# Kernel optimization log

Measured on AMD Instinct MI355X. Metric: run time of the kernel, lower is better.

The kernel has to match this reference:

```python
import jax, jax.numpy as jnp
import numpy as np

B, C, D = 16, 512, 256
K = 16        # spatio_topk
RD = 128      # rec_dim
H = 8         # num_heads
FFN = 1024    # temporal_ffn
TEMP = 0.5    # temperature


def setup_inputs() -> dict:
    key = jax.random.key(0)
    ks = jax.random.split(key, 8)
    s = lambda k, shape: (jax.random.normal(k, shape, jnp.float32) * 0.02)
    return dict(
        x=jax.random.normal(ks[0], (B, C, D), jnp.float32),
        wq_rec=s(ks[1], (RD, D)),
        wk_rec=s(ks[2], (RD, D)),
        in_proj_w=s(ks[3], (3 * D, D)),
        in_proj_b=jnp.zeros((3 * D,), jnp.float32),
        out_w=s(ks[4], (D, D)),
        out_b=jnp.zeros((D,), jnp.float32),
        ln1_g=jnp.ones((D,), jnp.float32),
        ln1_b=jnp.zeros((D,), jnp.float32),
        mlp_w1=s(ks[5], (FFN, D)),
        mlp_b1=jnp.zeros((FFN,), jnp.float32),
        mlp_w2=s(ks[6], (D, FFN)),
        mlp_b2=jnp.zeros((D,), jnp.float32),
        ln2_g=jnp.ones((D,), jnp.float32),
        ln2_b=jnp.zeros((D,), jnp.float32),
    )


def _ln(x, g, b, eps=1e-5):
    m = x.mean(-1, keepdims=True)
    v = ((x - m) ** 2).mean(-1, keepdims=True)
    return (x - m) * jax.lax.rsqrt(v + eps) * g + b


def reference(x, wq_rec, wk_rec, in_proj_w, in_proj_b, out_w, out_b,
              ln1_g, ln1_b, mlp_w1, mlp_b1, mlp_w2, mlp_b2, ln2_g, ln2_b):
    b, c, d = x.shape
    # --- ST_Rec_Module (training branch: straight-through top-k routing) ---
    xq = x @ wq_rec.T                                   # (B,C,RD)
    xk = x @ wk_rec.T
    logits = jnp.einsum('bqd,bkd->bqk', xq, xk) / TEMP  # (B,C,C)
    idx = jax.lax.top_k(logits, K)[1]                   # (B,C,K)
    z_hard = jax.nn.one_hot(idx, c, dtype=x.dtype)      # (B,C,K,C)
    # cumulative mask of previously-selected channels (exclusive cumsum)
    prev = jnp.cumsum(z_hard, axis=2)
    prev = jnp.concatenate([jnp.zeros_like(prev[:, :, :1]), prev[:, :, :-1]], axis=2)
    mask = prev > 0
    zs = jnp.where(mask, -1e30, logits[:, :, None, :] / TEMP)  # logits/temp twice, as in source
    z_soft = jax.nn.softmax(zs, axis=-1)
    z = z_hard + z_soft - jax.lax.stop_gradient(z_soft)        # straight-through
    rec_x = jnp.einsum('bqkc,bcd->bqkd', z, x)                 # (B,C,K,D)

    # --- ST_Channel_Module: per-channel cross-attention, query length 1 ---
    hd = d // H
    wq, wk, wv = in_proj_w[:d], in_proj_w[d:2 * d], in_proj_w[2 * d:]
    bq, bk, bv = in_proj_b[:d], in_proj_b[d:2 * d], in_proj_b[2 * d:]
    q = (x @ wq.T + bq).reshape(b, c, H, hd)                   # (B,C,H,hd)
    k = (rec_x @ wk.T + bk).reshape(b, c, K, H, hd)
    v = (rec_x @ wv.T + bv).reshape(b, c, K, H, hd)
    scores = jnp.einsum('bchd,bckhd->bchk', q, k) / np.float32(np.sqrt(hd))
    attn = jax.nn.softmax(scores, axis=-1)
    ctx = jnp.einsum('bchk,bckhd->bchd', attn, v).reshape(b, c, d)
    attn_out = ctx @ out_w.T + out_b
    x1 = _ln(attn_out + x, ln1_g, ln1_b)

    # --- ST_Temporal_Module (Identity projections, gelu FFN + LN) ---
    h = jax.nn.gelu(x1 @ mlp_w1.T + mlp_b1, approximate=False)
    h = h @ mlp_w2.T + mlp_b2
    x2 = _ln(h + x1, ln2_g, ln2_b)
    return x2
```

## Files before the change

### kernel.cpp

```cpp
#include <hip/hip_runtime.h>
#include <hip/hip_bf16.h>
#include <math.h>

#define B_   16
#define C_   512
#define D_   256
#define K_   16
#define RD_  128
#define H_   8
#define HD_  32
#define FFN_ 1024
#define M_   (B_ * C_)

typedef __attribute__((ext_vector_type(8))) short bf16x8;
typedef __attribute__((ext_vector_type(4))) float f32x4;

typedef __attribute__((address_space(1))) const int ga_int;
typedef __attribute__((address_space(3))) int ls_int;

static __device__ __forceinline__ short f2bf(float v) {
    __hip_bfloat16 h = __float2bfloat16(v);
    return *(short*)&h;
}
static __device__ __forceinline__ float bf2f(short s) {
    __hip_bfloat16 h = *(__hip_bfloat16*)&s;
    return __bfloat162float(h);
}
static __device__ __forceinline__ float4 ld4bf(const short* p) {
    uint2 u = *(const uint2*)p;
    float4 r;
    r.x = __uint_as_float((u.x & 0xffffu) << 16);
    r.y = __uint_as_float(u.x & 0xffff0000u);
    r.z = __uint_as_float((u.y & 0xffffu) << 16);
    r.w = __uint_as_float(u.y & 0xffff0000u);
    return r;
}

#define N8_X    (M_ * D_ / 8)
#define N8_INW  (768 * D_ / 8)
#define N8_OUTW (D_ * D_ / 8)
#define N8_W1   (FFN_ * D_ / 8)
#define N8_W2   (D_ * FFN_ / 8)
#define N8_WQ   (RD_ * D_ / 8)
#define N8_ALL  (N8_X + N8_INW + N8_OUTW + N8_W1 + N8_W2 + 2 * N8_WQ)

__global__ __launch_bounds__(256) void convert_all_kernel(
    const float* __restrict__ x, const float* __restrict__ inw,
    const float* __restrict__ outw, const float* __restrict__ w1,
    const float* __restrict__ w2, const float* __restrict__ wq,
    const float* __restrict__ wk,
    short* __restrict__ xbf, short* __restrict__ xlo,
    short* __restrict__ inwbf, short* __restrict__ outwbf,
    short* __restrict__ w1bf, short* __restrict__ w2bf,
    short* __restrict__ wqh, short* __restrict__ wql,
    short* __restrict__ wkh, short* __restrict__ wkl)
{
    int i = blockIdx.x * 256 + threadIdx.x;
    if (i >= N8_ALL) return;

    const float* s; short* dh; short* dl = nullptr; int off;
    if      (i < N8_X)                    { s = x;    dh = xbf;    dl = xlo; off = i; }
    else if (i < N8_X + N8_INW)           { s = inw;  dh = inwbf;  off = i - N8_X; }
    else if (i < N8_X + N8_INW + N8_OUTW) { s = outw; dh = outwbf; off = i - N8_X - N8_INW; }
    else if (i < N8_X + N8_INW + N8_OUTW + N8_W1)
                                          { s = w1;   dh = w1bf;   off = i - N8_X - N8_INW - N8_OUTW; }
    else if (i < N8_X + N8_INW + N8_OUTW + N8_W1 + N8_W2)
                                          { s = w2;   dh = w2bf;   off = i - N8_X - N8_INW - N8_OUTW - N8_W1; }
    else if (i < N8_X + N8_INW + N8_OUTW + N8_W1 + N8_W2 + N8_WQ)
                                          { s = wq;   dh = wqh; dl = wql; off = i - N8_X - N8_INW - N8_OUTW - N8_W1 - N8_W2; }
    else                                  { s = wk;   dh = wkh; dl = wkl; off = i - N8_X - N8_INW - N8_OUTW - N8_W1 - N8_W2 - N8_WQ; }

    const float4* sp = (const float4*)s + (size_t)off * 2;
    float4 v0 = sp[0], v1 = sp[1];
    float f[8] = {v0.x, v0.y, v0.z, v0.w, v1.x, v1.y, v1.z, v1.w};
    short rh[8], rl[8];
    #pragma unroll
    for (int j = 0; j < 8; ++j) {
        rh[j] = f2bf(f[j]);
        rl[j] = f2bf(f[j] - bf2f(rh[j]));
    }
    *(bf16x8*)(dh + (size_t)off * 8) = *(bf16x8*)rh;
    if (dl) *(bf16x8*)(dl + (size_t)off * 8) = *(bf16x8*)rl;
}

template<int BM, int BN, int OUT_BF16, int ACT>
__global__ __launch_bounds__(256) void gemm_mfma(
    const short* __restrict__ A, const short* __restrict__ W,
    const float* __restrict__ bias, void* __restrict__ Cout,
    int M, int N, int Kd)
{
    __shared__ short As[2][BM * 32];
    __shared__ short Bs[2][BN * 32];
    const int tid  = threadIdx.x;
    const int wave = tid >> 6;
    const int lane = tid & 63;
    const int bm = blockIdx.y * BM;
    const int bn = blockIdx.x * BN;
    constexpr int MI = BM / 32;
    constexpr int NJ = BN / 32;
    const int wr = (wave >> 1) * (BM / 2);
    const int wc = (wave & 1) * (BN / 2);

    const int fr = lane & 15;
    const int fk = (lane >> 4) * 8;
    const int r0 = tid >> 2, ch = (tid & 3) * 8;

    f32x4 acc[MI][NJ];
    #pragma unroll
    for (int i = 0; i < MI; ++i)
        #pragma unroll
        for (int j = 0; j < NJ; ++j)
            acc[i][j] = (f32x4){0.f, 0.f, 0.f, 0.f};

    auto stage = [&](int buf, int k0) {
        #pragma unroll
        for (int i = 0; i < BM / 64; ++i)
            __builtin_amdgcn_global_load_lds(
                (ga_int*)&A[(size_t)(bm + r0 + i * 64) * Kd + k0 + ch],
                (ls_int*)&As[buf][(tid + i * 256) * 8], 16, 0, 0);
        #pragma unroll
        for (int j = 0; j < BN / 64; ++j)
            __builtin_amdgcn_global_load_lds(
                (ga_int*)&W[(size_t)(bn + r0 + j * 64) * Kd + k0 + ch],
                (ls_int*)&Bs[buf][(tid + j * 256) * 8], 16, 0, 0);
    };

    stage(0, 0);
    int cur = 0;

    for (int k0 = 0; k0 < Kd; k0 += 32) {
        __syncthreads();
        if (k0 + 32 < Kd) stage(cur ^ 1, k0 + 32);

        bf16x8 af[MI], bfr[NJ];
        #pragma unroll
        for (int i = 0; i < MI; ++i) af[i]  = *(bf16x8*)&As[cur][(wr + i * 16 + fr) * 32 + fk];
        #pragma unroll
        for (int j = 0; j < NJ; ++j) bfr[j] = *(bf16x8*)&Bs[cur][(wc + j * 16 + fr) * 32 + fk];
        #pragma unroll
        for (int i = 0; i < MI; ++i)
            #pragma unroll
            for (int j = 0; j < NJ; ++j)
                acc[i][j] = __builtin_amdgcn_mfma_f32_16x16x32_bf16(af[i], bfr[j], acc[i][j], 0, 0, 0);
        cur ^= 1;
    }

    const int rowbase = (lane >> 4) * 4;
    #pragma unroll
    for (int i = 0; i < MI; ++i) {
        #pragma unroll
        for (int j = 0; j < NJ; ++j) {
            const int n = bn + wc + j * 16 + fr;
            const float bn_v = bias ? bias[n] : 0.f;
            #pragma unroll
            for (int r = 0; r < 4; ++r) {
                const int m = bm + wr + i * 16 + rowbase + r;
                float v = acc[i][j][r] + bn_v;
                if (ACT) v = 0.5f * v * (1.0f + erff(v * 0.70710678118654752f));
                if (OUT_BF16) ((short*)Cout)[(size_t)m * N + n] = f2bf(v);
                else          ((float*)Cout)[(size_t)m * N + n] = v;
            }
        }
    }
}

__global__ __launch_bounds__(256) void proj_kernel(
    const short* __restrict__ xbf, const short* __restrict__ xlo,
    const short* __restrict__ inwbf, const float* __restrict__ in_b,
    const short* __restrict__ wqh, const short* __restrict__ wql,
    const short* __restrict__ wkh, const short* __restrict__ wkl,
    short* __restrict__ qkvbf,
    short* __restrict__ qh, short* __restrict__ ql,
    short* __restrict__ kh, short* __restrict__ kl)
{
    __shared__ short smem[12288];
    const int bid  = blockIdx.x;
    const int tid  = threadIdx.x;
    const int wave = tid >> 6;
    const int lane = tid & 63;
    const int fr = lane & 15;
    const int fk = (lane >> 4) * 8;
    const int r0 = tid >> 2, ch = (tid & 3) * 8;

    if (bid < 768) {
        const int bm = (bid / 6) * 64;
        const int bn = (bid % 6) * 128;
        const int wr = (wave >> 1) * 32;
        const int wc = (wave & 1) * 64;
        short* As = smem;
        short* Bs = smem + 4096;

        f32x4 acc[2][4];
        #pragma unroll
        for (int i = 0; i < 2; ++i)
            #pragma unroll
            for (int j = 0; j < 4; ++j)
                acc[i][j] = (f32x4){0.f, 0.f, 0.f, 0.f};

        auto stage = [&](int buf, int k0) {
            __builtin_amdgcn_global_load_lds(
                (ga_int*)&xbf[(size_t)(bm + r0) * D_ + k0 + ch],
                (ls_int*)&As[buf * 2048 + tid * 8], 16, 0, 0);
            #pragma unroll
            for (int j = 0; j < 2; ++j)
                __builtin_amdgcn_global_load_lds(
                    (ga_int*)&inwbf[(size_t)(bn + r0 + j * 64) * D_ + k0 + ch],
                    (ls_int*)&Bs[buf * 4096 + (tid + j * 256) * 8], 16, 0, 0);
        };

        stage(0, 0);
        int cur = 0;
        for (int k0 = 0; k0 < D_; k0 += 32) {
            __syncthreads();
            if (k0 + 32 < D_) stage(cur ^ 1, k0 + 32);
            bf16x8 af[2], bfr[4];
            #pragma unroll
            for (int i = 0; i < 2; ++i) af[i]  = *(bf16x8*)&As[cur * 2048 + (wr + i * 16 + fr) * 32 + fk];
            #pragma unroll
            for (int j = 0; j < 4; ++j) bfr[j] = *(bf16x8*)&Bs[cur * 4096 + (wc + j * 16 + fr) * 32 + fk];
            #pragma unroll
            for (int i = 0; i < 2; ++i)
                #pragma unroll
                for (int j = 0; j < 4; ++j)
                    acc[i][j] = __builtin_amdgcn_mfma_f32_16x16x32_bf16(af[i], bfr[j], acc[i][j], 0, 0, 0);
            cur ^= 1;
        }

        const int rowbase = (lane >> 4) * 4;
        #pragma unroll
        for (int i = 0; i < 2; ++i)
            #pragma unroll
            for (int j = 0; j < 4; ++j) {
                const int n = bn + wc + j * 16 + fr;
                const float bv = in_b[n];
                #pragma unroll
                for (int r = 0; r < 4; ++r) {
                    const int m = bm + wr + i * 16 + rowbase + r;
                    qkvbf[(size_t)m * 768 + n] = f2bf(acc[i][j][r] + bv);
                }
            }
    } else {
        const int t = bid - 768;
        const int z = t >> 8;
        const int rem = t & 255;
        const int bm = (rem >> 1) * 64;
        const int bn = (rem & 1) * 64;
        const short* Wh = z ? wkh : wqh;
        const short* Wl = z ? wkl : wql;
        short* Oh = z ? kh : qh;
        short* Ol = z ? kl : ql;
        short* Ah = smem;
        short* Al = smem + 2048;
        short* Bh = smem + 4096;
        short* Bl = smem + 6144;

        const int wr = (wave >> 1) * 32;
        const int wc = (wave & 1) * 32;

        f32x4 acc[2][2];
        #pragma unroll
        for (int i = 0; i < 2; ++i)
            #pragma unroll
            for (int j = 0; j < 2; ++j)
                acc[i][j] = (f32x4){0.f, 0.f, 0.f, 0.f};

        for (int k0 = 0; k0 < D_; k0 += 32) {
            __builtin_amdgcn_global_load_lds((ga_int*)&xbf[(size_t)(bm + r0) * D_ + k0 + ch], (ls_int*)&Ah[tid * 8], 16, 0, 0);
            __builtin_amdgcn_global_load_lds((ga_int*)&xlo[(size_t)(bm + r0) * D_ + k0 + ch], (ls_int*)&Al[tid * 8], 16, 0, 0);
            __builtin_amdgcn_global_load_lds((ga_int*)&Wh[(size_t)(bn + r0) * D_ + k0 + ch], (ls_int*)&Bh[tid * 8], 16, 0, 0);
            __builtin_amdgcn_global_load_lds((ga_int*)&Wl[(size_t)(bn + r0) * D_ + k0 + ch], (ls_int*)&Bl[tid * 8], 16, 0, 0);
            __syncthreads();

            bf16x8 ah[2], al[2], bh[2], bl[2];
            #pragma unroll
            for (int i = 0; i < 2; ++i) {
                ah[i] = *(bf16x8*)&Ah[(wr + i * 16 + fr) * 32 + fk];
                al[i] = *(bf16x8*)&Al[(wr + i * 16 + fr) * 32 + fk];
            }
            #pragma unroll
            for (int j = 0; j < 2; ++j) {
                bh[j] = *(bf16x8*)&Bh[(wc + j * 16 + fr) * 32 + fk];
                bl[j] = *(bf16x8*)&Bl[(wc + j * 16 + fr) * 32 + fk];
            }
            #pragma unroll
            for (int i = 0; i < 2; ++i)
                #pragma unroll
                for (int j = 0; j < 2; ++j) {
                    acc[i][j] = __builtin_amdgcn_mfma_f32_16x16x32_bf16(ah[i], bh[j], acc[i][j], 0, 0, 0);
                    acc[i][j] = __builtin_amdgcn_mfma_f32_16x16x32_bf16(ah[i], bl[j], acc[i][j], 0, 0, 0);
                    acc[i][j] = __builtin_amdgcn_mfma_f32_16x16x32_bf16(al[i], bh[j], acc[i][j], 0, 0, 0);
                }
            __syncthreads();
        }

        const int rowbase = (lane >> 4) * 4;
        #pragma unroll
        for (int i = 0; i < 2; ++i)
            #pragma unroll
            for (int j = 0; j < 2; ++j) {
                const int n = bn + wc + j * 16 + fr;
                #pragma unroll
                for (int r = 0; r < 4; ++r) {
                    const int m = bm + wr + i * 16 + rowbase + r;
                    float v = acc[i][j][r];
                    short h = f2bf(v);
                    Oh[(size_t)m * RD_ + n] = h;
                    Ol[(size_t)m * RD_ + n] = f2bf(v - bf2f(h));
                }
            }
    }
}

__global__ __launch_bounds__(256) void logits_mfma(
    const short* __restrict__ qh, const short* __restrict__ ql,
    const short* __restrict__ kh, const short* __restrict__ kl,
    float* __restrict__ out)
{
    __shared__ short Ah[64 * 32], Al[64 * 32], Bh[64 * 32], Bl[64 * 32];
    const int tid  = threadIdx.x;
    const int wave = tid >> 6;
    const int lane = tid & 63;
    const int base = blockIdx.z * C_;
    const int bm = blockIdx.y * 64;
    const int bn = blockIdx.x * 64;
    const int wr = (wave >> 1) * 32;
    const int wc = (wave & 1) * 32;
    const int fr = lane & 15;
    const int fk = (lane >> 4) * 8;
    const int r0 = tid >> 2, ch = (tid & 3) * 8;

    f32x4 acc[2][2];
    #pragma unroll
    for (int i = 0; i < 2; ++i)
        #pragma unroll
        for (int j = 0; j < 2; ++j)
            acc[i][j] = (f32x4){0.f, 0.f, 0.f, 0.f};

    for (int k0 = 0; k0 < RD_; k0 += 32) {
        __builtin_amdgcn_global_load_lds((ga_int*)&qh[(size_t)(base + bm + r0) * RD_ + k0 + ch], (ls_int*)&Ah[tid * 8], 16, 0, 0);
        __builtin_amdgcn_global_load_lds((ga_int*)&ql[(size_t)(base + bm + r0) * RD_ + k0 + ch], (ls_int*)&Al[tid * 8], 16, 0, 0);
        __builtin_amdgcn_global_load_lds((ga_int*)&kh[(size_t)(base + bn + r0) * RD_ + k0 + ch], (ls_int*)&Bh[tid * 8], 16, 0, 0);
        __builtin_amdgcn_global_load_lds((ga_int*)&kl[(size_t)(base + bn + r0) * RD_ + k0 + ch], (ls_int*)&Bl[tid * 8], 16, 0, 0);
        __syncthreads();

        bf16x8 ah[2], al[2], bh[2], bl[2];
        #pragma unroll
        for (int i = 0; i < 2; ++i) {
            ah[i] = *(bf16x8*)&Ah[(wr + i * 16 + fr) * 32 + fk];
            al[i] = *(bf16x8*)&Al[(wr + i * 16 + fr) * 32 + fk];
        }
        #pragma unroll
        for (int j = 0; j < 2; ++j) {
            bh[j] = *(bf16x8*)&Bh[(wc + j * 16 + fr) * 32 + fk];
            bl[j] = *(bf16x8*)&Bl[(wc + j * 16 + fr) * 32 + fk];
        }
        #pragma unroll
        for (int i = 0; i < 2; ++i)
            #pragma unroll
            for (int j = 0; j < 2; ++j) {
                acc[i][j] = __builtin_amdgcn_mfma_f32_16x16x32_bf16(ah[i], bh[j], acc[i][j], 0, 0, 0);
                acc[i][j] = __builtin_amdgcn_mfma_f32_16x16x32_bf16(ah[i], bl[j], acc[i][j], 0, 0, 0);
                acc[i][j] = __builtin_amdgcn_mfma_f32_16x16x32_bf16(al[i], bh[j], acc[i][j], 0, 0, 0);
            }
        __syncthreads();
    }

    const int rowbase = (lane >> 4) * 4;
    #pragma unroll
    for (int i = 0; i < 2; ++i)
        #pragma unroll
        for (int j = 0; j < 2; ++j) {
            const int n = bn + wc + j * 16 + fr;
            #pragma unroll
            for (int r = 0; r < 4; ++r) {
                const int m = base + bm + wr + i * 16 + rowbase + r;
                out[(size_t)m * C_ + n] = acc[i][j][r];
            }
        }
}

__global__ __launch_bounds__(256) void attn_ln_kernel(
    const float* __restrict__ logits, const short* __restrict__ qkv,
    const short* __restrict__ W, const float* __restrict__ bias,
    const float* __restrict__ res, const float* __restrict__ g,
    const float* __restrict__ beta,
    float* __restrict__ out, short* __restrict__ outbf)
{
    __shared__ short ctxlds[16 * 256];
    __shared__ short Bs[2][256 * 32];
    __shared__ float part[4][16][2];

    const int tid  = threadIdx.x;
    const int wave = tid >> 6;
    const int lane = tid & 63;
    const int bm = blockIdx.x * 16;
    const int wc = wave * 64;
    const int fr = lane & 15;
    const int fk = (lane >> 4) * 8;
    const int r0 = tid >> 2, ch = (tid & 3) * 8;

    auto stageB = [&](int buf, int k0) {
        #pragma unroll
        for (int j = 0; j < 4; ++j)
            __builtin_amdgcn_global_load_lds(
                (ga_int*)&W[(size_t)(r0 + j * 64) * D_ + k0 + ch],
                (ls_int*)&Bs[buf][(tid + j * 256) * 8], 16, 0, 0);
    };

    stageB(0, 0);

    for (int rq = 0; rq < 4; ++rq) {
        const int lrow_i = bm + wave * 4 + rq;
        const int bbase = lrow_i & ~(C_ - 1);
        const float* lrow = logits + (size_t)lrow_i * C_;

        float v[8];
        #pragma unroll
        for (int j = 0; j < 8; ++j) v[j] = lrow[lane * 8 + j];

        int ii[K_];
        #pragma unroll
        for (int sel = 0; sel < K_; ++sel) {
            float bv = v[0]; int bj = 0;
            #pragma unroll
            for (int j = 1; j < 8; ++j)
                if (v[j] > bv) { bv = v[j]; bj = j; }
            float wb = bv;
            #pragma unroll
            for (int s = 1; s < 64; s <<= 1)
                wb = fmaxf(wb, __shfl_xor(wb, s, 64));
            unsigned long long mask = __ballot(bv == wb);
            int wl = __ffsll(mask) - 1;
            int wj = __shfl(bj, wl, 64);
            ii[sel] = wl * 8 + wj;
            #pragma unroll
            for (int j = 0; j < 8; ++j)
                if (lane == wl && bj == j) v[j] = -INFINITY;
        }

        float4 qv = ld4bf(qkv + (size_t)lrow_i * 768 + lane * 4);

        float s[K_];
        #pragma unroll
        for (int k = 0; k < K_; ++k) {
            float4 kv = ld4bf(qkv + (size_t)(bbase + ii[k]) * 768 + 256 + lane * 4);
            float p = qv.x * kv.x + qv.y * kv.y + qv.z * kv.z + qv.w * kv.w;
            p += __shfl_xor(p, 1, 64);
            p += __shfl_xor(p, 2, 64);
            p += __shfl_xor(p, 4, 64);
            s[k] = p * 0.17677669529663687f;
        }

        float m = s[0];
        #pragma unroll
        for (int k = 1; k < K_; ++k) m = fmaxf(m, s[k]);
        float ssum = 0.f;
        #pragma unroll
        for (int k = 0; k < K_; ++k) { s[k] = __expf(s[k] - m); ssum += s[k]; }
        const float inv = 1.f / ssum;

        float4 acc4 = {0.f, 0.f, 0.f, 0.f};
        #pragma unroll
        for (int k = 0; k < K_; ++k) {
            float4 vvv = ld4bf(qkv + (size_t)(bbase + ii[k]) * 768 + 512 + lane * 4);
            float w = s[k] * inv;
            acc4.x += w * vvv.x; acc4.y += w * vvv.y; acc4.z += w * vvv.z; acc4.w += w * vvv.w;
        }

        unsigned lo = (unsigned)(unsigned short)f2bf(acc4.x) | ((unsigned)(unsigned short)f2bf(acc4.y) << 16);
        unsigned hi = (unsigned)(unsigned short)f2bf(acc4.z) | ((unsigned)(unsigned short)f2bf(acc4.w) << 16);
        uint2 pk = {lo, hi};
        const int c0 = lane * 4;
        *(uint2*)&ctxlds[(c0 >> 5) * 512 + (wave * 4 + rq) * 32 + (c0 & 31)] = pk;
    }

    f32x4 acc[4];
    #pragma unroll
    for (int j = 0; j < 4; ++j) acc[j] = (f32x4){0.f, 0.f, 0.f, 0.f};

    int cur = 0;
    for (int k0 = 0; k0 < D_; k0 += 32) {
        __syncthreads();
        if (k0 + 32 < D_) stageB(cur ^ 1, k0 + 32);

        bf16x8 af = *(bf16x8*)&ctxlds[(k0 >> 5) * 512 + fr * 32 + fk];
        bf16x8 bfr[4];
        #pragma unroll
        for (int j = 0; j < 4; ++j) bfr[j] = *(bf16x8*)&Bs[cur][(wc + j * 16 + fr) * 32 + fk];
        #pragma unroll
        for (int j = 0; j < 4; ++j)
            acc[j] = __builtin_amdgcn_mfma_f32_16x16x32_bf16(af, bfr[j], acc[j], 0, 0, 0);
        cur ^= 1;
    }

    const int rowbase = (lane >> 4) * 4;
    float vv[4][4];
    float sum[4] = {0.f, 0.f, 0.f, 0.f};
    float sq[4]  = {0.f, 0.f, 0.f, 0.f};

    #pragma unroll
    for (int j = 0; j < 4; ++j) {
        const int n = wc + j * 16 + fr;
        const float bv = bias[n];
        #pragma unroll
        for (int r = 0; r < 4; ++r) {
            const int m = bm + rowbase + r;
            float v = acc[j][r] + bv + res[(size_t)m * D_ + n];
            vv[j][r] = v;
            sum[r] += v;
            sq[r]  += v * v;
        }
    }

    #pragma unroll
    for (int r = 0; r < 4; ++r)
        #pragma unroll
        for (int s = 1; s < 16; s <<= 1) {
            sum[r] += __shfl_xor(sum[r], s, 64);
            sq[r]  += __shfl_xor(sq[r],  s, 64);
        }

    if (fr == 0) {
        #pragma unroll
        for (int r = 0; r < 4; ++r) {
            part[wave][rowbase + r][0] = sum[r];
            part[wave][rowbase + r][1] = sq[r];
        }
    }
    __syncthreads();

    #pragma unroll
    for (int r = 0; r < 4; ++r) {
        const int ml = rowbase + r;
        const float S = part[0][ml][0] + part[1][ml][0] + part[2][ml][0] + part[3][ml][0];
        const float Q = part[0][ml][1] + part[1][ml][1] + part[2][ml][1] + part[3][ml][1];
        const float mean = S * (1.0f / D_);
        const float var  = Q * (1.0f / D_) - mean * mean;
        const float rstd = rsqrtf(var + 1e-5f);
        const int m = bm + ml;
        #pragma unroll
        for (int j = 0; j < 4; ++j) {
            const int n = wc + j * 16 + fr;
            float o = (vv[j][r] - mean) * rstd * g[n] + beta[n];
            out[(size_t)m * D_ + n] = o;
            outbf[(size_t)m * D_ + n] = f2bf(o);
        }
    }
}

template<int KD, int WBF>
__global__ __launch_bounds__(256) void gemm_ln_mfma(
    const short* __restrict__ A, const short* __restrict__ W,
    const float* __restrict__ bias, const float* __restrict__ res,
    const float* __restrict__ g, const float* __restrict__ beta,
    float* __restrict__ out, short* __restrict__ outbf)
{
    __shared__ short As[2][16 * 32];
    __shared__ short Bs[2][256 * 32];
    __shared__ float part[4][16][2];

    const int tid  = threadIdx.x;
    const int wave = tid >> 6;
    const int lane = tid & 63;
    const int bm = blockIdx.x * 16;
    const int wc = wave * 64;
    const int fr = lane & 15;
    const int fk = (lane >> 4) * 8;
    const int r0 = tid >> 2, ch = (tid & 3) * 8;

    f32x4 acc[4];
    #pragma unroll
    for (int j = 0; j < 4; ++j) acc[j] = (f32x4){0.f, 0.f, 0.f, 0.f};

    auto stage = [&](int buf, int k0) {
        if (tid < 64)
            __builtin_amdgcn_global_load_lds(
                (ga_int*)&A[(size_t)(bm + r0) * KD + k0 + ch],
                (ls_int*)&As[buf][tid * 8], 16, 0, 0);
        #pragma unroll
        for (int j = 0; j < 4; ++j)
            __builtin_amdgcn_global_load_lds(
                (ga_int*)&W[(size_t)(r0 + j * 64) * KD + k0 + ch],
                (ls_int*)&Bs[buf][(tid + j * 256) * 8], 16, 0, 0);
    };

    stage(0, 0);
    int cur = 0;

    for (int k0 = 0; k0 < KD; k0 += 32) {
        __syncthreads();
        if (k0 + 32 < KD) stage(cur ^ 1, k0 + 32);

        bf16x8 af = *(bf16x8*)&As[cur][fr * 32 + fk];
        bf16x8 bfr[4];
        #pragma unroll
        for (int j = 0; j < 4; ++j) bfr[j] = *(bf16x8*)&Bs[cur][(wc + j * 16 + fr) * 32 + fk];
        #pragma unroll
        for (int j = 0; j < 4; ++j)
            acc[j] = __builtin_amdgcn_mfma_f32_16x16x32_bf16(af, bfr[j], acc[j], 0, 0, 0);
        cur ^= 1;
    }

    const int rowbase = (lane >> 4) * 4;
    float vv[4][4];
    float sum[4] = {0.f, 0.f, 0.f, 0.f};
    float sq[4]  = {0.f, 0.f, 0.f, 0.f};

    #pragma unroll
    for (int j = 0; j < 4; ++j) {
        const int n = wc + j * 16 + fr;
        const float bv = bias[n];
        #pragma unroll
        for (int r = 0; r < 4; ++r) {
            const int m = bm + rowbase + r;
            float v = acc[j][r] + bv + res[(size_t)m * D_ + n];
            vv[j][r] = v;
            sum[r] += v;
            sq[r]  += v * v;
        }
    }

    #pragma unroll
    for (int r = 0; r < 4; ++r)
        #pragma unroll
        for (int s = 1; s < 16; s <<= 1) {
            sum[r] += __shfl_xor(sum[r], s, 64);
            sq[r]  += __shfl_xor(sq[r],  s, 64);
        }

    if (fr == 0) {
        #pragma unroll
        for (int r = 0; r < 4; ++r) {
            part[wave][rowbase + r][0] = sum[r];
            part[wave][rowbase + r][1] = sq[r];
        }
    }
    __syncthreads();

    #pragma unroll
    for (int r = 0; r < 4; ++r) {
        const int ml = rowbase + r;
        const float S = part[0][ml][0] + part[1][ml][0] + part[2][ml][0] + part[3][ml][0];
        const float Q = part[0][ml][1] + part[1][ml][1] + part[2][ml][1] + part[3][ml][1];
        const float mean = S * (1.0f / D_);
        const float var  = Q * (1.0f / D_) - mean * mean;
        const float rstd = rsqrtf(var + 1e-5f);
        const int m = bm + ml;
        #pragma unroll
        for (int j = 0; j < 4; ++j) {
            const int n = wc + j * 16 + fr;
            float o = (vv[j][r] - mean) * rstd * g[n] + beta[n];
            out[(size_t)m * D_ + n] = o;
            if (WBF) outbf[(size_t)m * D_ + n] = f2bf(o);
        }
    }
}

extern "C" void kernel_launch(void* const* d_in, const int* in_sizes, int n_in,
                              void* d_out, int out_size, void* d_ws, size_t ws_size,
                              hipStream_t stream)
{
    const float* x      = (const float*)d_in[0];
    const float* wq_rec = (const float*)d_in[1];
    const float* wk_rec = (const float*)d_in[2];
    const float* in_w   = (const float*)d_in[3];
    const float* in_b   = (const float*)d_in[4];
    const float* out_w  = (const float*)d_in[5];
    const float* out_b  = (const float*)d_in[6];
    const float* ln1_g  = (const float*)d_in[7];
    const float* ln1_b  = (const float*)d_in[8];
    const float* w1     = (const float*)d_in[9];
    const float* b1     = (const float*)d_in[10];
    const float* w2     = (const float*)d_in[11];
    const float* b2     = (const float*)d_in[12];
    const float* ln2_g  = (const float*)d_in[13];
    const float* ln2_b  = (const float*)d_in[14];
    float* out = (float*)d_out;

    short* qkvbf = (short*)d_ws;
    short* qh    = qkvbf + (size_t)M_ * 768;
    short* ql    = qh + (size_t)M_ * RD_;
    short* kh    = ql + (size_t)M_ * RD_;
    short* kl    = kh + (size_t)M_ * RD_;
    float* x1    = (float*)(kl + (size_t)M_ * RD_);
    float* U     = x1 + (size_t)M_ * D_;
    float* logits = U;
    short* x1bf   = (short*)(U + (size_t)M_ * 512);
    short* hbf    = x1bf  + (size_t)M_ * D_;
    short* xbf    = hbf   + (size_t)M_ * FFN_;
    short* xlo    = xbf   + (size_t)M_ * D_;
    short* inwbf  = xlo   + (size_t)M_ * D_;
    short* outwbf = inwbf + (size_t)768 * D_;
    short* w1bf   = outwbf + (size_t)D_ * D_;
    short* w2bf   = w1bf  + (size_t)FFN_ * D_;
    short* wqh    = w2bf  + (size_t)D_ * FFN_;
    short* wql    = wqh + (size_t)RD_ * D_;
    short* wkh    = wql + (size_t)RD_ * D_;
    short* wkl    = wkh + (size_t)RD_ * D_;

    dim3 blk(256);

    convert_all_kernel<<<dim3((N8_ALL + 255) / 256), blk, 0, stream>>>(
        x, in_w, out_w, w1, w2, wq_rec, wk_rec,
        xbf, xlo, inwbf, outwbf, w1bf, w2bf, wqh, wql, wkh, wkl);

    proj_kernel<<<dim3(1280), blk, 0, stream>>>(
        xbf, xlo, inwbf, in_b, wqh, wql, wkh, wkl, qkvbf, qh, ql, kh, kl);
    logits_mfma<<<dim3(C_ / 64, C_ / 64, B_), blk, 0, stream>>>(qh, ql, kh, kl, logits);
    attn_ln_kernel<<<dim3(M_ / 16), blk, 0, stream>>>(
        logits, qkvbf, outwbf, out_b, x, ln1_g, ln1_b, x1, x1bf);
    gemm_mfma<64, 128, 1, 1><<<dim3(FFN_ / 128, M_ / 64), blk, 0, stream>>>(x1bf, w1bf, b1, hbf, M_, FFN_, D_);
    gemm_ln_mfma<1024, 0><<<dim3(M_ / 16), blk, 0, stream>>>(
        hbf, w2bf, b2, x1, ln2_g, ln2_b, out, nullptr);
}
```

Baseline: 111.7 us.

## Split top-k selection into its own kernel and single-buffer attention weight staging

Top-k routing over the logits moves out of the attention/out-projection/LN kernel into a separate kernel, with one wavefront per row across M/4 blocks. That kernel writes 16-bit indices to workspace, which the attention kernel then reads. The attention kernel also switches from double to single buffering of the weight tile, which cuts shared memory but adds a second barrier per k-step. Block indices are swizzled so that neighbouring blocks cover different batches. The aim is more parallelism and occupancy for the serial top-k work, at the cost of an extra launch, an index round trip through memory, and less load/compute overlap.

```diff
diff --git a/kernel.cpp b/kernel.cpp
--- a/kernel.cpp
+++ b/kernel.cpp
@@ -379,66 +379,81 @@
         }
 }
 
-__global__ __launch_bounds__(256) void attn_ln_kernel(
-    const float* __restrict__ logits, const short* __restrict__ qkv,
+__global__ __launch_bounds__(256) void topk_select_kernel(
+    const float* __restrict__ logits, unsigned short* __restrict__ idx16)
+{
+    const int wave = threadIdx.x >> 6;
+    const int lane = threadIdx.x & 63;
+    const int row  = blockIdx.x * 4 + wave;
+    const float* lrow = logits + (size_t)row * C_;
+
+    float v[8];
+    #pragma unroll
+    for (int j = 0; j < 8; ++j) v[j] = lrow[lane * 8 + j];
+
+    unsigned short my = 0;
+    #pragma unroll
+    for (int sel = 0; sel < K_; ++sel) {
+        float bv = v[0]; int bj = 0;
+        #pragma unroll
+        for (int j = 1; j < 8; ++j)
+            if (v[j] > bv) { bv = v[j]; bj = j; }
+        float wb = bv;
+        #pragma unroll
+        for (int s = 1; s < 64; s <<= 1)
+            wb = fmaxf(wb, __shfl_xor(wb, s, 64));
+        unsigned long long mask = __ballot(bv == wb);
+        int wl = __ffsll(mask) - 1;
+        int wj = __shfl(bj, wl, 64);
+        if (lane == sel) my = (unsigned short)(wl * 8 + wj);
+        #pragma unroll
+        for (int j = 0; j < 8; ++j)
+            if (lane == wl && bj == j) v[j] = -INFINITY;
+    }
+    if (lane < K_) idx16[(size_t)row * K_ + lane] = my;
+}
+
+__global__ __launch_bounds__(256) void attnproj_ln_kernel(
+    const unsigned short* __restrict__ idx16, const short* __restrict__ qkv,
     const short* __restrict__ W, const float* __restrict__ bias,
     const float* __restrict__ res, const float* __restrict__ g,
     const float* __restrict__ beta,
     float* __restrict__ out, short* __restrict__ outbf)
 {
     __shared__ short ctxlds[16 * 256];
-    __shared__ short Bs[2][256 * 32];
+    __shared__ short Bs[256 * 32];
     __shared__ float part[4][16][2];
 
+    const int bid = ((blockIdx.x & 7) << 6) + (blockIdx.x >> 3);
     const int tid  = threadIdx.x;
     const int wave = tid >> 6;
     const int lane = tid & 63;
-    const int bm = blockIdx.x * 16;
+    const int bm = bid * 16;
     const int wc = wave * 64;
     const int fr = lane & 15;
     const int fk = (lane >> 4) * 8;
     const int r0 = tid >> 2, ch = (tid & 3) * 8;
 
-    auto stageB = [&](int buf, int k0) {
+    auto stageB = [&](int k0) {
         #pragma unroll
         for (int j = 0; j < 4; ++j)
             __builtin_amdgcn_global_load_lds(
                 (ga_int*)&W[(size_t)(r0 + j * 64) * D_ + k0 + ch],
-                (ls_int*)&Bs[buf][(tid + j * 256) * 8], 16, 0, 0);
+                (ls_int*)&Bs[(tid + j * 256) * 8], 16, 0, 0);
     };
 
-    stageB(0, 0);
+    stageB(0);
 
     for (int rq = 0; rq < 4; ++rq) {
-        const int lrow_i = bm + wave * 4 + rq;
-        const int bbase = lrow_i & ~(C_ - 1);
-        const float* lrow = logits + (size_t)lrow_i * C_;
-
-        float v[8];
-        #pragma unroll
-        for (int j = 0; j < 8; ++j) v[j] = lrow[lane * 8 + j];
+        const int row = bm + wave * 4 + rq;
+        const int bbase = row & ~(C_ - 1);
+        const unsigned short* ip = idx16 + (size_t)row * K_;
 
         int ii[K_];
         #pragma unroll
-        for (int sel = 0; sel < K_; ++sel) {
-            float bv = v[0]; int bj = 0;
-            #pragma unroll
-            for (int j = 1; j < 8; ++j)
-                if (v[j] > bv) { bv = v[j]; bj = j; }
-            float wb = bv;
-            #pragma unroll
-            for (int s = 1; s < 64; s <<= 1)
-                wb = fmaxf(wb, __shfl_xor(wb, s, 64));
-            unsigned long long mask = __ballot(bv == wb);
-            int wl = __ffsll(mask) - 1;
-            int wj = __shfl(bj, wl, 64);
-            ii[sel] = wl * 8 + wj;
-            #pragma unroll
-            for (int j = 0; j < 8; ++j)
-                if (lane == wl && bj == j) v[j] = -INFINITY;
-        }
-
-        float4 qv = ld4bf(qkv + (size_t)lrow_i * 768 + lane * 4);
+        for (int k = 0; k < K_; ++k) ii[k] = ip[k];
+
+        float4 qv = ld4bf(qkv + (size_t)row * 768 + lane * 4);
 
         float s[K_];
         #pragma unroll
@@ -478,19 +493,19 @@
     #pragma unroll
     for (int j = 0; j < 4; ++j) acc[j] = (f32x4){0.f, 0.f, 0.f, 0.f};
 
-    int cur = 0;
     for (int k0 = 0; k0 < D_; k0 += 32) {
         __syncthreads();
-        if (k0 + 32 < D_) stageB(cur ^ 1, k0 + 32);
 
         bf16x8 af = *(bf16x8*)&ctxlds[(k0 >> 5) * 512 + fr * 32 + fk];
         bf16x8 bfr[4];
         #pragma unroll
-        for (int j = 0; j < 4; ++j) bfr[j] = *(bf16x8*)&Bs[cur][(wc + j * 16 + fr) * 32 + fk];
+        for (int j = 0; j < 4; ++j) bfr[j] = *(bf16x8*)&Bs[(wc + j * 16 + fr) * 32 + fk];
         #pragma unroll
         for (int j = 0; j < 4; ++j)
             acc[j] = __builtin_amdgcn_mfma_f32_16x16x32_bf16(af, bfr[j], acc[j], 0, 0, 0);
-        cur ^= 1;
+
+        __syncthreads();
+        if (k0 + 32 < D_) stageB(k0 + 32);
     }
 
     const int rowbase = (lane >> 4) * 4;
@@ -685,7 +700,8 @@
     float* x1    = (float*)(kl + (size_t)M_ * RD_);
     float* U     = x1 + (size_t)M_ * D_;
     float* logits = U;
-    short* x1bf   = (short*)(U + (size_t)M_ * 512);
+    unsigned short* idx16 = (unsigned short*)(U + (size_t)M_ * 512);
+    short* x1bf   = (short*)idx16 + (size_t)M_ * D_;
     short* hbf    = x1bf  + (size_t)M_ * D_;
     short* xbf    = hbf   + (size_t)M_ * FFN_;
     short* xlo    = xbf   + (size_t)M_ * D_;
@@ -707,8 +723,9 @@
     proj_kernel<<<dim3(1280), blk, 0, stream>>>(
         xbf, xlo, inwbf, in_b, wqh, wql, wkh, wkl, qkvbf, qh, ql, kh, kl);
     logits_mfma<<<dim3(C_ / 64, C_ / 64, B_), blk, 0, stream>>>(qh, ql, kh, kl, logits);
-    attn_ln_kernel<<<dim3(M_ / 16), blk, 0, stream>>>(
-        logits, qkvbf, outwbf, out_b, x, ln1_g, ln1_b, x1, x1bf);
+    topk_select_kernel<<<dim3(M_ / 4), blk, 0, stream>>>(logits, idx16);
+    attnproj_ln_kernel<<<dim3(M_ / 16), blk, 0, stream>>>(
+        idx16, qkvbf, outwbf, out_b, x, ln1_g, ln1_b, x1, x1bf);
     gemm_mfma<64, 128, 1, 1><<<dim3(FFN_ / 128, M_ / 64), blk, 0, stream>>>(x1bf, w1bf, b1, hbf, M_, FFN_, D_);
     gemm_ln_mfma<1024, 0><<<dim3(M_ / 16), blk, 0, stream>>>(
         hbf, w2bf, b2, x1, ln2_g, ln2_b, out, nullptr);
```

After: 115.9 us. +3.8%, slower.
